# Performance work log

Measured on AMD Instinct MI355X. Metric: run time of the kernel, lower is better.

## Reference

```python
import jax, jax.numpy as jnp
import numpy as np

IMG = 512
B = 4
NA = 3          # anchors per location
NC = 3          # classes
K = 512         # pre-NMS top-k per image per level (<= smallest level anchor count 768)
STRIDES = [4, 8, 16, 32]
MIN_S = [0.01, 0.02, 0.03, 0.04]
MAX_S = [0.06, 0.08, 0.10, 0.12]
W_SC = [0.8, 0.9, 1.0, 1.1]
H_SC = [1.0, 1.2, 1.4, 1.6]
CONF_T = 0.15
NMS_T = 0.5
STD = 0.2       # box_delta_stds (means are 0)


def make_anchors(stride):
    H = IMG // stride
    c = (np.arange(H) + 0.5) * stride
    cy, cx = np.meshgrid(c, c, indexing='ij')           # [H, W]
    sizes = stride * 4.0 * (2.0 ** (np.arange(NA) / 3.0))  # [A]
    cx = np.broadcast_to(cx, (NA, H, H))
    cy = np.broadcast_to(cy, (NA, H, H))
    s = sizes[:, None, None]
    # A-major, then H, W -- matches permute(0,1,3,4,2).reshape flattening
    anc = np.stack([cx - s / 2, cy - s / 2, cx + s / 2, cy + s / 2], -1).reshape(-1, 4)
    return jnp.asarray(anc, jnp.float32)


def setup_inputs() -> dict:
    key = jax.random.key(0)
    ks = jax.random.split(key, 8)
    inp = {}
    for l, s in enumerate(STRIDES):
        H = IMG // s
        inp[f'cls{l}'] = jax.random.normal(ks[2 * l], (B, NA, NC, H, H), jnp.float32)
        inp[f'box{l}'] = jax.random.normal(ks[2 * l + 1], (B, NA, 4, H, H), jnp.float32)
        inp[f'anc{l}'] = make_anchors(s)
    inp['image_size'] = IMG
    return inp


def decode_level(cls, box, anc, lvl, image_size):
    Bc, A, C, H, W = cls.shape
    scores = jax.nn.sigmoid(jnp.transpose(cls, (0, 1, 3, 4, 2)).reshape(Bc, -1, C))  # [B,N,C]
    d = jnp.transpose(box, (0, 1, 3, 4, 2)).reshape(Bc, -1, 4)                        # [B,N,4]
    img = jnp.asarray(image_size, jnp.float32)
    aw = (anc[:, 2] - anc[:, 0]) / img
    ah = (anc[:, 3] - anc[:, 1]) / img
    acx = (anc[:, 0] + anc[:, 2]) * 0.5 / img
    acy = (anc[:, 1] + anc[:, 3]) * 0.5 / img
    fs = 1.0 / STRIDES[lvl]
    dx = jnp.clip(d[..., 0] * STD, -1.0, 1.0) * fs * aw
    dy = jnp.clip(d[..., 1] * STD, -1.0, 1.0) * fs * ah
    cx = jnp.clip(acx + dx, 0.0, 1.0)
    cy = jnp.clip(acy + dy, 0.0, 1.0)
    dw = jnp.clip(d[..., 2] * STD, -2.0, 2.0)
    dh = jnp.clip(d[..., 3] * STD, -2.0, 2.0)
    pw = jnp.clip(aw * W_SC[lvl] * jnp.exp(dw * (0.2 + 0.1 * lvl)), MIN_S[lvl] * 0.8, MAX_S[lvl] * 0.9)
    ph = jnp.clip(ah * H_SC[lvl] * jnp.exp(dh * (0.4 + 0.2 * lvl)), MIN_S[lvl] * 0.8, MAX_S[lvl] * 1.2)
    boxes = jnp.stack([
        jnp.clip(cx - 0.5 * pw, 0.0, 1.0),
        jnp.clip(cy - 0.5 * ph, 0.0, 1.0),
        jnp.clip(cx + 0.5 * pw, 0.0, 1.0),
        jnp.clip(cy + 0.5 * ph, 0.0, 1.0)], -1)                                       # [B,N,4]
    ms = scores.max(-1)
    mc = scores.argmax(-1)
    w = boxes[..., 2] - boxes[..., 0]
    h = boxes[..., 3] - boxes[..., 1]
    valid = (ms > CONF_T) & (w > MIN_S[lvl] * 0.5) & (h > MIN_S[lvl] * 0.5) \
            & (w < MAX_S[lvl] * 2.0) & (h < MAX_S[lvl] * 2.0)
    # pre-NMS top-k on (masked) scores
    sort_key = jnp.where(valid, ms, -1.0)
    _, idx = jax.lax.top_k(sort_key, K)                                               # [B,K]
    boxes_k = jnp.take_along_axis(boxes, idx[..., None], 1)
    scores_k = jnp.take_along_axis(ms, idx, 1)
    labels_k = jnp.take_along_axis(mc, idx, 1)
    valid_k = jnp.take_along_axis(valid, idx, 1)
    return boxes_k, scores_k, labels_k, valid_k


def pairwise_iou(b):
    area = (b[:, 2] - b[:, 0]) * (b[:, 3] - b[:, 1])
    lt = jnp.maximum(b[:, None, :2], b[None, :, :2])
    rb = jnp.minimum(b[:, None, 2:], b[None, :, 2:])
    wh = jnp.clip(rb - lt, 0.0)
    inter = wh[..., 0] * wh[..., 1]
    return inter / (area[:, None] + area[None, :] - inter + 1e-9)


def nms_keep(boxes, valid):
    # boxes sorted by descending score; sequential greedy NMS
    iou = pairwise_iou(boxes)                 # [K,K]
    rank = jnp.arange(K)
    def body(i, keep):
        overlap = jnp.max(jnp.where((rank < i) & keep, iou[i], 0.0))
        return keep.at[i].set(valid[i] & (overlap <= NMS_T))
    return jax.lax.fori_loop(0, K, body, jnp.zeros((K,), bool))


def reference(cls0, box0, anc0, cls1, box1, anc1, cls2, box2, anc2, cls3, box3, anc3, image_size):
    levels = [(cls0, box0, anc0), (cls1, box1, anc1), (cls2, box2, anc2), (cls3, box3, anc3)]
    outs = [decode_level(c, b, a, l, image_size) for l, (c, b, a) in enumerate(levels)]
    boxes = jnp.stack([o[0] for o in outs], 1)    # [B, L, K, 4]
    scores = jnp.stack([o[1] for o in outs], 1)   # [B, L, K]
    labels = jnp.stack([o[2] for o in outs], 1)   # [B, L, K]
    valid = jnp.stack([o[3] for o in outs], 1)    # [B, L, K]
    keep = jax.vmap(jax.vmap(nms_keep))(boxes, valid)
    boxes = jnp.where(keep[..., None], boxes, 0.0)
    scores = jnp.where(keep, scores, 0.0)
    labels = jnp.where(keep, labels + 1, 0)       # torch code returns labels + 1
    return boxes, scores, labels, keep
```

## Files before the change

kernel.cpp:

```cpp
#include <hip/hip_runtime.h>
#include <math.h>

#define K_TOP 512
#define CAND_CAP 3072

struct LvlC {
  int H, lgH, HH, lgHH;
  float fs, wsc, hsc, wex, hex, pwlo, pwhi, phlo, phhi, minwh, maxwh;
};

__device__ const LvlC LVL[4] = {
  {128, 7, 16384, 14, 0.25f,    0.8f, 1.0f, 0.2f, 0.4f, 0.008f, 0.054f, 0.008f, 0.072f, 0.005f, 0.12f},
  { 64, 6,  4096, 12, 0.125f,   0.9f, 1.2f, 0.3f, 0.6f, 0.016f, 0.072f, 0.016f, 0.096f, 0.01f,  0.16f},
  { 32, 5,  1024, 10, 0.0625f,  1.0f, 1.4f, 0.4f, 0.8f, 0.024f, 0.09f,  0.024f, 0.12f,  0.015f, 0.2f },
  { 16, 4,   256,  8, 0.03125f, 1.1f, 1.6f, 0.5f, 1.0f, 0.032f, 0.108f, 0.032f, 0.144f, 0.02f,  0.24f},
};

__device__ const float TSEL[4] = {0.91f, 0.85f, 0.65f, -2.0f};

__device__ __forceinline__ void decode_box(const LvlC& L, const float* __restrict__ boxp,
                                           const float* __restrict__ ancp,
                                           int b, int idx, float rimg,
                                           float& x0, float& y0, float& x1, float& y1)
{
#pragma clang fp contract(off)
  int a   = idx >> L.lgHH;
  int rem = idx & (L.HH - 1);
  const float* bp = boxp + (size_t)((b * 3 + a) * 4) * L.HH + rem;
  float d0 = bp[0], d1 = bp[L.HH], d2 = bp[2 * L.HH], d3 = bp[3 * L.HH];
  float4 av = reinterpret_cast<const float4*>(ancp)[idx];
  float a0 = av.x, a1 = av.y, a2 = av.z, a3 = av.w;
  float aw  = (a2 - a0) * rimg;
  float ah  = (a3 - a1) * rimg;
  float acx = (a0 + a2) * 0.5f * rimg;
  float acy = (a1 + a3) * 0.5f * rimg;
  float dx = fminf(fmaxf(d0 * 0.2f, -1.f), 1.f) * L.fs * aw;
  float dy = fminf(fmaxf(d1 * 0.2f, -1.f), 1.f) * L.fs * ah;
  float cx = fminf(fmaxf(acx + dx, 0.f), 1.f);
  float cy = fminf(fmaxf(acy + dy, 0.f), 1.f);
  float dw = fminf(fmaxf(d2 * 0.2f, -2.f), 2.f);
  float dh = fminf(fmaxf(d3 * 0.2f, -2.f), 2.f);
  float pw = fminf(fmaxf(aw * L.wsc * expf(dw * L.wex), L.pwlo), L.pwhi);
  float ph = fminf(fmaxf(ah * L.hsc * expf(dh * L.hex), L.phlo), L.phhi);
  x0 = fminf(fmaxf(cx - 0.5f * pw, 0.f), 1.f);
  y0 = fminf(fmaxf(cy - 0.5f * ph, 0.f), 1.f);
  x1 = fminf(fmaxf(cx + 0.5f * pw, 0.f), 1.f);
  y1 = fminf(fmaxf(cy + 0.5f * ph, 0.f), 1.f);
}

__device__ __forceinline__ void seg_map(int blk, int& b, int& l, int& base, int& iblk)
{
  b = blk / 255;
  int rb = blk - b * 255;
  if (rb < 192)      { l = 0; iblk = rb;       base = 0;     }
  else if (rb < 240) { l = 1; iblk = rb - 192; base = 49152; }
  else if (rb < 252) { l = 2; iblk = rb - 240; base = 61440; }
  else               { l = 3; iblk = rb - 252; base = 64512; }
}

__global__ __launch_bounds__(256) void dc_kernel(
    const float* __restrict__ cls0, const float* __restrict__ box0, const float* __restrict__ anc0,
    const float* __restrict__ cls1, const float* __restrict__ box1, const float* __restrict__ anc1,
    const float* __restrict__ cls2, const float* __restrict__ box2, const float* __restrict__ anc2,
    const float* __restrict__ cls3, const float* __restrict__ box3, const float* __restrict__ anc3,
    const int* __restrict__ imgp, unsigned long long* __restrict__ keys,
    unsigned long long* __restrict__ cand, unsigned* __restrict__ unitCnt)
{
  __shared__ unsigned wcnt[4];
  int unit = (int)blockIdx.x;
  int tid = (int)threadIdx.x;
  int wid = tid >> 6, lane = tid & 63;
  int b, l, base, iblk;
  seg_map(unit, b, l, base, iblk);
  int i = iblk * 256 + tid;

  const float *cls, *boxp, *ancp;
  switch (l) {
    case 0:  cls = cls0; boxp = box0; ancp = anc0; break;
    case 1:  cls = cls1; boxp = box1; ancp = anc1; break;
    case 2:  cls = cls2; boxp = box2; ancp = anc2; break;
    default: cls = cls3; boxp = box3; ancp = anc3; break;
  }
  LvlC L = LVL[l];
  float rimg = 1.0f / (float)(*imgp);

  int a   = i >> L.lgHH;
  int rem = i & (L.HH - 1);
  const float* cp = cls + (size_t)((b * 3 + a) * 3) * L.HH + rem;
  float c0 = cp[0], c1 = cp[L.HH], c2 = cp[2 * L.HH];
  float m = c0; int mc = 0;
  if (c1 > m) { m = c1; mc = 1; }
  if (c2 > m) { m = c2; mc = 2; }
  float ms = 1.f / (1.f + expf(-m));

  float x0, y0, x1, y1;
  decode_box(L, boxp, ancp, b, i, rimg, x0, y0, x1, y1);
  float w = x1 - x0, h = y1 - y0;
  bool valid = (ms > 0.15f) && (w > L.minwh) && (h > L.minwh) && (w < L.maxwh) && (h < L.maxwh);

  float sk = valid ? ms : -1.0f;
  unsigned u = __float_as_uint(sk);
  unsigned ascu  = (u & 0x80000000u) ? ~u : (u | 0x80000000u);
  unsigned descu = ~ascu;
  unsigned long long key = ((unsigned long long)descu << 32)
                         | ((unsigned long long)(unsigned)i << 16)
                         | ((unsigned)mc << 8) | (valid ? 1u : 0u);
  keys[(size_t)b * 65280 + base + i] = key;

  bool take = (sk >= TSEL[l]);
  unsigned long long bm = __ballot(take);
  if (lane == 0) wcnt[wid] = (unsigned)__popcll(bm);
  __syncthreads();
  if (take) {
    unsigned off = 0;
    for (int w2 = 0; w2 < wid; ++w2) off += wcnt[w2];
    off += (unsigned)__popcll(bm & ((1ull << lane) - 1ull));
    cand[(size_t)unit * 256 + off] = key;
  }
  if (tid == 0) unitCnt[unit] = wcnt[0] + wcnt[1] + wcnt[2] + wcnt[3];
}

__global__ __launch_bounds__(512) void sel_kernel(
    const unsigned long long* __restrict__ keys,
    const unsigned long long* __restrict__ cand, const unsigned* __restrict__ unitCnt,
    const float* __restrict__ box0, const float* __restrict__ anc0,
    const float* __restrict__ box1, const float* __restrict__ anc1,
    const float* __restrict__ box2, const float* __restrict__ anc2,
    const float* __restrict__ box3, const float* __restrict__ anc3,
    const int* __restrict__ imgp,
    float* __restrict__ boxesWS, float* __restrict__ scoresWS,
    int* __restrict__ labelsWS, unsigned* __restrict__ validWS)
{
  __shared__ unsigned long long scand[CAND_CAP];
  __shared__ unsigned long long skey[K_TOP];
  __shared__ unsigned long long skey2[K_TOP];
  __shared__ unsigned hist[8][256];
  __shared__ unsigned upref[256];
  __shared__ unsigned waveSum[8];
  __shared__ unsigned long long shPrefix;
  __shared__ unsigned long long shKth;
  __shared__ unsigned shBelow, shCnt, shTotal, shBucketCnt, sBC;

  int seg = (int)blockIdx.x;
  int b = seg >> 2, l = seg & 3;
  int tid = (int)threadIdx.x;
  const int nt = 512;
  int wid = tid >> 6, lane = tid & 63;

  const int nArr[4]    = {49152, 12288, 3072, 768};
  const int baseArr[4] = {0, 49152, 61440, 64512};
  const int nuArr[4]   = {192, 48, 12, 3};
  const int fuArr[4]   = {0, 192, 240, 252};
  int N = nArr[l];
  int nu = nuArr[l];
  int firstU = b * 255 + fuArr[l];
  const unsigned long long* kp = keys + (size_t)b * 65280 + baseArr[l];

  if (tid == 0) { shPrefix = 0ull; shBelow = 0u; shCnt = 0u; sBC = 0u; shBucketCnt = 0xFFFFFFFFu; }

  unsigned c = (tid < nu) ? unitCnt[firstU + tid] : 0u;
  unsigned incl = c;
  for (int off = 1; off < 64; off <<= 1) {
    unsigned n = __shfl_up(incl, off);
    if (lane >= off) incl += n;
  }
  if (lane == 63) waveSum[wid] = incl;
  __syncthreads();
  if (tid < 256) {
    unsigned add = 0;
    for (int w2 = 0; w2 < wid; ++w2) add += waveSum[w2];
    if (tid < nu) upref[tid] = incl - c + add;
  }
  if (tid == 0) shTotal = waveSum[0] + waveSum[1] + waveSum[2] + waveSum[3];
  __syncthreads();

  unsigned total = shTotal;
  bool useCand = (total >= K_TOP && total <= CAND_CAP);
  int M = useCand ? (int)total : N;

  if (useCand) {
    for (int f = tid; f < (int)total; f += nt) {
      int lo = 0, hi = nu - 1;
      while (lo < hi) {
        int mid = (lo + hi + 1) >> 1;
        if ((int)upref[mid] <= f) lo = mid; else hi = mid - 1;
      }
      scand[f] = cand[(size_t)(firstU + lo) * 256 + (unsigned)(f - (int)upref[lo])];
    }
  }
  __syncthreads();

  int lastShift = 16;
  for (int r = 0; r < 6; ++r) {
    int shift = 56 - 8 * r;
    for (int v = tid; v < 8 * 256; v += nt) ((unsigned*)hist)[v] = 0u;
    __syncthreads();
    unsigned long long pref = shPrefix;
    unsigned below = shBelow;
    unsigned long long hiMask = (r == 0) ? 0ull : (~0ull << (64 - 8 * r));
    for (int t = tid; t < M; t += nt) {
      unsigned long long k = useCand ? scand[t] : kp[t];
      if ((k & hiMask) == (pref & hiMask))
        atomicAdd(&hist[wid][(unsigned)((k >> shift) & 0xFF)], 1u);
    }
    __syncthreads();
    unsigned s = 0, incl2 = 0;
    if (tid < 256) {
#pragma unroll
      for (int w2 = 0; w2 < 8; ++w2) s += hist[w2][tid];
      incl2 = s;
    }
    for (int off = 1; off < 64; off <<= 1) {
      unsigned n = __shfl_up(incl2, off);
      if (lane >= off) incl2 += n;
    }
    if (lane == 63) waveSum[wid] = incl2;
    __syncthreads();
    if (tid < 256) {
      unsigned add = 0;
      for (int w2 = 0; w2 < wid; ++w2) add += waveSum[w2];
      unsigned inclT = incl2 + add;
      unsigned exclT = inclT - s;
      if (below + exclT < K_TOP && below + inclT >= K_TOP) {
        shBelow = below + exclT;
        shPrefix = pref | ((unsigned long long)(unsigned)tid << shift);
        shBucketCnt = s;
      }
    }
    __syncthreads();
    if (shBucketCnt <= (unsigned)K_TOP) { lastShift = shift; break; }
  }

  {
    unsigned long long pmask = ~0ull << lastShift;
    unsigned long long pref = shPrefix;
    for (int t = tid; t < M; t += nt) {
      unsigned long long k = useCand ? scand[t] : kp[t];
      bool take = ((k & pmask) == pref);
      unsigned long long bm = __ballot(take);
      unsigned bp = 0;
      if (lane == 0 && bm) bp = atomicAdd(&sBC, (unsigned)__popcll(bm));
      bp = __shfl(bp, 0);
      if (take) skey[bp + (unsigned)__popcll(bm & ((1ull << lane) - 1ull))] = k;
    }
    __syncthreads();
    unsigned cnt = sBC;
    unsigned rneed = K_TOP - shBelow;
    if (tid < (int)cnt) {
      unsigned long long mykey = skey[tid];
      int rank = 0;
      for (unsigned j = 0; j < cnt; ++j) rank += (skey[j] < mykey) ? 1 : 0;
      if (rank == (int)(rneed - 1)) shKth = mykey;
    }
    __syncthreads();
  }
  unsigned long long kth = shKth;

  for (int t = tid; t < M; t += nt) {
    unsigned long long k = useCand ? scand[t] : kp[t];
    bool take = (k <= kth);
    unsigned long long bm = __ballot(take);
    unsigned bp = 0;
    if (lane == 0 && bm) bp = atomicAdd(&shCnt, (unsigned)__popcll(bm));
    bp = __shfl(bp, 0);
    if (take) skey[bp + (unsigned)__popcll(bm & ((1ull << lane) - 1ull))] = k;
  }
  __syncthreads();

  {
    unsigned long long mykey = skey[tid];
    int rank = 0;
#pragma unroll 8
    for (int j = 0; j < K_TOP; ++j) rank += (skey[j] < mykey) ? 1 : 0;
    skey2[rank] = mykey;
  }
  __syncthreads();

  const float *boxp, *ancp;
  switch (l) {
    case 0:  boxp = box0; ancp = anc0; break;
    case 1:  boxp = box1; ancp = anc1; break;
    case 2:  boxp = box2; ancp = anc2; break;
    default: boxp = box3; ancp = anc3; break;
  }
  LvlC L = LVL[l];
  float rimg = 1.0f / (float)(*imgp);
  {
    unsigned long long key = skey2[tid];
    int idx = (int)((key >> 16) & 0xFFFFull);
    unsigned descu = (unsigned)(key >> 32);
    unsigned ascu  = ~descu;
    unsigned u = (ascu & 0x80000000u) ? (ascu & 0x7FFFFFFFu) : ~ascu;
    float x0, y0, x1, y1;
    decode_box(L, boxp, ancp, b, idx, rimg, x0, y0, x1, y1);
    int o = seg * K_TOP + tid;
    float4 bb; bb.x = x0; bb.y = y0; bb.z = x1; bb.w = y1;
    reinterpret_cast<float4*>(boxesWS)[o] = bb;
    scoresWS[o] = __uint_as_float(u);
    labelsWS[o] = (int)((key >> 8) & 0xFFull);
    validWS[o]  = (unsigned)(key & 1ull);
  }
}

__global__ __launch_bounds__(256) void mask_kernel(
    const float* __restrict__ boxesWS, unsigned long long* __restrict__ masks)
{
#pragma clang fp contract(off)
  int blk = (int)blockIdx.x;
  int seg = blk >> 5;
  int wid = (int)threadIdx.x >> 6;
  int lane = (int)threadIdx.x & 63;
  int waveInSeg = (blk & 31) * 4 + wid;
  const float4* bb = reinterpret_cast<const float4*>(boxesWS) + seg * K_TOP;
  unsigned long long* mseg = masks + (size_t)seg * K_TOP * 8;

  float4 bj[8]; float aj[8];
#pragma unroll
  for (int c = 0; c < 8; ++c) {
    bj[c] = bb[c * 64 + lane];
    aj[c] = (bj[c].z - bj[c].x) * (bj[c].w - bj[c].y);
  }
#pragma unroll
  for (int rr = 0; rr < 4; ++rr) {
    int r = waveInSeg * 4 + rr;
    float4 br = bb[r];
    float ar_ = (br.z - br.x) * (br.w - br.y);
#pragma unroll
    for (int c = 0; c < 8; ++c) {
      float ltx = fmaxf(br.x, bj[c].x), lty = fmaxf(br.y, bj[c].y);
      float rbx = fminf(br.z, bj[c].z), rby = fminf(br.w, bj[c].w);
      float ww = fmaxf(rbx - ltx, 0.f), hh = fmaxf(rby - lty, 0.f);
      float inter = ww * hh;
      float iou = inter / (ar_ + aj[c] - inter + 1e-9f);
      unsigned long long bal = __ballot(iou > 0.5f);
      if (lane == 0) mseg[c * K_TOP + r] = bal;
    }
  }
}

__global__ __launch_bounds__(512) void scan_kernel(
    const unsigned long long* __restrict__ masks,
    const float* __restrict__ boxesWS, const float* __restrict__ scoresWS,
    const int* __restrict__ labelsWS, const unsigned* __restrict__ validWS,
    float* __restrict__ out)
{
  __shared__ unsigned long long sMaskT[8 * K_TOP];
  __shared__ unsigned long long keepWords[8];
  __shared__ unsigned sChanged;

  int seg = (int)blockIdx.x;
  int tid = (int)threadIdx.x;
  int wid = tid >> 6, lane = tid & 63;
  const unsigned long long* mp = masks + (size_t)seg * K_TOP * 8;
#pragma unroll
  for (int w = 0; w < 8; ++w) sMaskT[w * K_TOP + tid] = mp[w * K_TOP + tid];
  bool valid = validWS[seg * K_TOP + tid] != 0u;

  unsigned long long myWord = __ballot(valid);
  if (lane == 0) keepWords[wid] = myWord;
  __syncthreads();

  for (int it = 0; it < 513; ++it) {
    unsigned long long sup = 0ull;
    for (int w = 0; w < wid; ++w)
      sup |= sMaskT[w * K_TOP + tid] & keepWords[w];
    sup |= sMaskT[wid * K_TOP + tid] & keepWords[wid] & ((1ull << lane) - 1ull);
    bool nk = valid && (sup == 0ull);
    unsigned long long nw = __ballot(nk);
    __syncthreads();
    if (tid == 0) sChanged = 0u;
    __syncthreads();
    if (lane == 0) {
      if (nw != keepWords[wid]) sChanged = 1u;
      keepWords[wid] = nw;
    }
    __syncthreads();
    if (sChanged == 0u) break;
  }

  int o = seg * K_TOP + tid;
  bool keep = (keepWords[wid] >> lane) & 1ull;
  float4 bx = reinterpret_cast<const float4*>(boxesWS)[o];
  float4 ob;
  ob.x = keep ? bx.x : 0.f;
  ob.y = keep ? bx.y : 0.f;
  ob.z = keep ? bx.z : 0.f;
  ob.w = keep ? bx.w : 0.f;
  reinterpret_cast<float4*>(out)[o] = ob;
  out[32768 + o] = keep ? scoresWS[o] : 0.f;
  out[40960 + o] = keep ? (float)(labelsWS[o] + 1) : 0.f;
  out[49152 + o] = keep ? 1.f : 0.f;
}

extern "C" void kernel_launch(void* const* d_in, const int* in_sizes, int n_in,
                              void* d_out, int out_size, void* d_ws, size_t ws_size,
                              hipStream_t stream)
{
  const float* cls0 = (const float*)d_in[0];
  const float* box0 = (const float*)d_in[1];
  const float* anc0 = (const float*)d_in[2];
  const float* cls1 = (const float*)d_in[3];
  const float* box1 = (const float*)d_in[4];
  const float* anc1 = (const float*)d_in[5];
  const float* cls2 = (const float*)d_in[6];
  const float* box2 = (const float*)d_in[7];
  const float* anc2 = (const float*)d_in[8];
  const float* cls3 = (const float*)d_in[9];
  const float* box3 = (const float*)d_in[10];
  const float* anc3 = (const float*)d_in[11];
  const int*   imgp = (const int*)d_in[12];

  char* ws = (char*)d_ws;
  unsigned long long* keys    = (unsigned long long*)(ws + 0);
  unsigned long long* cand    = (unsigned long long*)(ws + 2088960);
  unsigned*           unitCnt = (unsigned*)(ws + 4177920);
  float*              boxesWS = (float*)(ws + 4182016);
  float*              scoresWS= (float*)(ws + 4313088);
  int*                labelsWS= (int*)(ws + 4345856);
  unsigned*           validWS = (unsigned*)(ws + 4378624);
  unsigned long long* masks   = (unsigned long long*)(ws + 4411392);
  float* out = (float*)d_out;

  dc_kernel<<<1020, 256, 0, stream>>>(cls0, box0, anc0, cls1, box1, anc1,
                                      cls2, box2, anc2, cls3, box3, anc3,
                                      imgp, keys, cand, unitCnt);
  sel_kernel<<<16, 512, 0, stream>>>(keys, cand, unitCnt,
                                     box0, anc0, box1, anc1, box2, anc2, box3, anc3,
                                     imgp, boxesWS, scoresWS, labelsWS, validWS);
  mask_kernel<<<512, 256, 0, stream>>>(boxesWS, masks);
  scan_kernel<<<16, 512, 0, stream>>>(masks, boxesWS, scoresWS, labelsWS, validWS, out);
}
```

Before: 116.2 us.

## Fuse select, mask and scan kernels into one launch with flag-based inter-block sync

Merges the selection, IoU-mask and greedy-scan kernels into a single persistent launch. Blocks 0-15 do top-k and box decode, publish a flag, then wait for 16 mask-builder blocks per segment before running the scan. Mask blocks spin on the per-segment flag with sleep and a bounded guard. Scores and labels stay in registers instead of a workspace round trip, and the scan loop uses double-buffered keep words to drop one barrier per iteration. This removes two kernel launch gaps but relies on all 272 blocks being co-resident, otherwise the spin-waits only end through their timeout guard.

```diff
diff --git a/kernel.cpp b/kernel.cpp
--- a/kernel.cpp
+++ b/kernel.cpp
@@ -64,12 +64,14 @@
     const float* __restrict__ cls2, const float* __restrict__ box2, const float* __restrict__ anc2,
     const float* __restrict__ cls3, const float* __restrict__ box3, const float* __restrict__ anc3,
     const int* __restrict__ imgp, unsigned long long* __restrict__ keys,
-    unsigned long long* __restrict__ cand, unsigned* __restrict__ unitCnt)
+    unsigned long long* __restrict__ cand, unsigned* __restrict__ unitCnt,
+    unsigned* __restrict__ flags)
 {
   __shared__ unsigned wcnt[4];
   int unit = (int)blockIdx.x;
   int tid = (int)threadIdx.x;
   int wid = tid >> 6, lane = tid & 63;
+  if (unit == 0 && tid < 64) flags[tid] = 0u;
   int b, l, base, iblk;
   seg_map(unit, b, l, base, iblk);
   int i = iblk * 256 + tid;
@@ -120,7 +122,7 @@
   if (tid == 0) unitCnt[unit] = wcnt[0] + wcnt[1] + wcnt[2] + wcnt[3];
 }
 
-__global__ __launch_bounds__(512) void sel_kernel(
+__global__ __launch_bounds__(512) void post_kernel(
     const unsigned long long* __restrict__ keys,
     const unsigned long long* __restrict__ cand, const unsigned* __restrict__ unitCnt,
     const float* __restrict__ box0, const float* __restrict__ anc0,
@@ -128,24 +130,72 @@
     const float* __restrict__ box2, const float* __restrict__ anc2,
     const float* __restrict__ box3, const float* __restrict__ anc3,
     const int* __restrict__ imgp,
-    float* __restrict__ boxesWS, float* __restrict__ scoresWS,
-    int* __restrict__ labelsWS, unsigned* __restrict__ validWS)
+    float* __restrict__ boxesWS, unsigned long long* __restrict__ masks,
+    unsigned* __restrict__ flags, float* __restrict__ out)
 {
-  __shared__ unsigned long long scand[CAND_CAP];
-  __shared__ unsigned long long skey[K_TOP];
-  __shared__ unsigned long long skey2[K_TOP];
-  __shared__ unsigned hist[8][256];
+  __shared__ alignas(16) char smem[40960];
+  unsigned long long* scand  = (unsigned long long*)(smem);
+  unsigned long long* skey   = (unsigned long long*)(smem + 24576);
+  unsigned long long* skey2  = (unsigned long long*)(smem + 28672);
+  unsigned (*hist)[256]      = (unsigned (*)[256])(smem + 32768);
+  unsigned long long* sMaskT = (unsigned long long*)(smem);
   __shared__ unsigned upref[256];
   __shared__ unsigned waveSum[8];
+  __shared__ unsigned long long keepW[2][8];
+  __shared__ unsigned cfl[2];
   __shared__ unsigned long long shPrefix;
   __shared__ unsigned long long shKth;
   __shared__ unsigned shBelow, shCnt, shTotal, shBucketCnt, sBC;
 
+  int tid = (int)threadIdx.x;
+  int wid = tid >> 6, lane = tid & 63;
+  const int nt = 512;
+
+  if (blockIdx.x >= 16) {
+#pragma clang fp contract(off)
+    int m = (int)blockIdx.x - 16;
+    int seg = m >> 4, sub = m & 15;
+    if (tid == 0) {
+      int guard = 0;
+      while (__hip_atomic_load(&flags[seg], __ATOMIC_ACQUIRE, __HIP_MEMORY_SCOPE_AGENT) == 0u) {
+        __builtin_amdgcn_s_sleep(2);
+        if (++guard > 4000000) break;
+      }
+    }
+    __syncthreads();
+    const float4* bb = reinterpret_cast<const float4*>(boxesWS) + seg * K_TOP;
+    unsigned long long* mseg = masks + (size_t)seg * K_TOP * 8;
+    int waveInSeg = sub * 8 + wid;
+    float4 bj[8]; float aj[8];
+#pragma unroll
+    for (int c = 0; c < 8; ++c) {
+      bj[c] = bb[c * 64 + lane];
+      aj[c] = (bj[c].z - bj[c].x) * (bj[c].w - bj[c].y);
+    }
+#pragma unroll
+    for (int rr = 0; rr < 4; ++rr) {
+      int r = waveInSeg * 4 + rr;
+      float4 br = bb[r];
+      float ar_ = (br.z - br.x) * (br.w - br.y);
+#pragma unroll
+      for (int c = 0; c < 8; ++c) {
+        float ltx = fmaxf(br.x, bj[c].x), lty = fmaxf(br.y, bj[c].y);
+        float rbx = fminf(br.z, bj[c].z), rby = fminf(br.w, bj[c].w);
+        float ww = fmaxf(rbx - ltx, 0.f), hh = fmaxf(rby - lty, 0.f);
+        float inter = ww * hh;
+        float iou = inter / (ar_ + aj[c] - inter + 1e-9f);
+        unsigned long long bal = __ballot(iou > 0.5f);
+        if (lane == 0) mseg[c * K_TOP + r] = bal;
+      }
+    }
+    __syncthreads();
+    if (tid == 0)
+      __hip_atomic_fetch_add(&flags[16 + seg], 1u, __ATOMIC_RELEASE, __HIP_MEMORY_SCOPE_AGENT);
+    return;
+  }
+
   int seg = (int)blockIdx.x;
   int b = seg >> 2, l = seg & 3;
-  int tid = (int)threadIdx.x;
-  const int nt = 512;
-  int wid = tid >> 6, lane = tid & 63;
 
   const int nArr[4]    = {49152, 12288, 3072, 768};
   const int baseArr[4] = {0, 49152, 61440, 64512};
@@ -285,110 +335,70 @@
   }
   LvlC L = LVL[l];
   float rimg = 1.0f / (float)(*imgp);
-  {
-    unsigned long long key = skey2[tid];
-    int idx = (int)((key >> 16) & 0xFFFFull);
-    unsigned descu = (unsigned)(key >> 32);
-    unsigned ascu  = ~descu;
-    unsigned u = (ascu & 0x80000000u) ? (ascu & 0x7FFFFFFFu) : ~ascu;
-    float x0, y0, x1, y1;
-    decode_box(L, boxp, ancp, b, idx, rimg, x0, y0, x1, y1);
-    int o = seg * K_TOP + tid;
-    float4 bb; bb.x = x0; bb.y = y0; bb.z = x1; bb.w = y1;
-    reinterpret_cast<float4*>(boxesWS)[o] = bb;
-    scoresWS[o] = __uint_as_float(u);
-    labelsWS[o] = (int)((key >> 8) & 0xFFull);
-    validWS[o]  = (unsigned)(key & 1ull);
-  }
-}
-
-__global__ __launch_bounds__(256) void mask_kernel(
-    const float* __restrict__ boxesWS, unsigned long long* __restrict__ masks)
-{
-#pragma clang fp contract(off)
-  int blk = (int)blockIdx.x;
-  int seg = blk >> 5;
-  int wid = (int)threadIdx.x >> 6;
-  int lane = (int)threadIdx.x & 63;
-  int waveInSeg = (blk & 31) * 4 + wid;
-  const float4* bb = reinterpret_cast<const float4*>(boxesWS) + seg * K_TOP;
-  unsigned long long* mseg = masks + (size_t)seg * K_TOP * 8;
-
-  float4 bj[8]; float aj[8];
-#pragma unroll
-  for (int c = 0; c < 8; ++c) {
-    bj[c] = bb[c * 64 + lane];
-    aj[c] = (bj[c].z - bj[c].x) * (bj[c].w - bj[c].y);
-  }
-#pragma unroll
-  for (int rr = 0; rr < 4; ++rr) {
-    int r = waveInSeg * 4 + rr;
-    float4 br = bb[r];
-    float ar_ = (br.z - br.x) * (br.w - br.y);
-#pragma unroll
-    for (int c = 0; c < 8; ++c) {
-      float ltx = fmaxf(br.x, bj[c].x), lty = fmaxf(br.y, bj[c].y);
-      float rbx = fminf(br.z, bj[c].z), rby = fminf(br.w, bj[c].w);
-      float ww = fmaxf(rbx - ltx, 0.f), hh = fmaxf(rby - lty, 0.f);
-      float inter = ww * hh;
-      float iou = inter / (ar_ + aj[c] - inter + 1e-9f);
-      unsigned long long bal = __ballot(iou > 0.5f);
-      if (lane == 0) mseg[c * K_TOP + r] = bal;
-    }
-  }
-}
-
-__global__ __launch_bounds__(512) void scan_kernel(
-    const unsigned long long* __restrict__ masks,
-    const float* __restrict__ boxesWS, const float* __restrict__ scoresWS,
-    const int* __restrict__ labelsWS, const unsigned* __restrict__ validWS,
-    float* __restrict__ out)
-{
-  __shared__ unsigned long long sMaskT[8 * K_TOP];
-  __shared__ unsigned long long keepWords[8];
-  __shared__ unsigned sChanged;
-
-  int seg = (int)blockIdx.x;
-  int tid = (int)threadIdx.x;
-  int wid = tid >> 6, lane = tid & 63;
+
+  unsigned long long key = skey2[tid];
+  int idx = (int)((key >> 16) & 0xFFFFull);
+  unsigned descu = (unsigned)(key >> 32);
+  unsigned ascu  = ~descu;
+  unsigned u = (ascu & 0x80000000u) ? (ascu & 0x7FFFFFFFu) : ~ascu;
+  int label = (int)((key >> 8) & 0xFFull);
+  bool valid = (key & 1ull) != 0ull;
+  float x0, y0, x1, y1;
+  decode_box(L, boxp, ancp, b, idx, rimg, x0, y0, x1, y1);
+  float4 mybox; mybox.x = x0; mybox.y = y0; mybox.z = x1; mybox.w = y1;
+  reinterpret_cast<float4*>(boxesWS)[seg * K_TOP + tid] = mybox;
+  __syncthreads();
+
+  if (tid == 0) {
+    __hip_atomic_fetch_add(&flags[seg], 1u, __ATOMIC_RELEASE, __HIP_MEMORY_SCOPE_AGENT);
+    int guard = 0;
+    while (__hip_atomic_load(&flags[16 + seg], __ATOMIC_ACQUIRE, __HIP_MEMORY_SCOPE_AGENT) < 16u) {
+      __builtin_amdgcn_s_sleep(2);
+      if (++guard > 4000000) break;
+    }
+  }
+  __syncthreads();
+
   const unsigned long long* mp = masks + (size_t)seg * K_TOP * 8;
 #pragma unroll
   for (int w = 0; w < 8; ++w) sMaskT[w * K_TOP + tid] = mp[w * K_TOP + tid];
-  bool valid = validWS[seg * K_TOP + tid] != 0u;
-
   unsigned long long myWord = __ballot(valid);
-  if (lane == 0) keepWords[wid] = myWord;
-  __syncthreads();
-
-  for (int it = 0; it < 513; ++it) {
+  if (lane == 0) keepW[0][wid] = myWord;
+  __syncthreads();
+
+  int p = 0;
+  for (int it = 0; it < 600; ++it) {
+    unsigned long long kws[8];
+#pragma unroll
+    for (int w = 0; w < 8; ++w) kws[w] = keepW[p][w];
     unsigned long long sup = 0ull;
     for (int w = 0; w < wid; ++w)
-      sup |= sMaskT[w * K_TOP + tid] & keepWords[w];
-    sup |= sMaskT[wid * K_TOP + tid] & keepWords[wid] & ((1ull << lane) - 1ull);
+      sup |= sMaskT[w * K_TOP + tid] & kws[w];
+    sup |= sMaskT[wid * K_TOP + tid] & kws[wid] & ((1ull << lane) - 1ull);
     bool nk = valid && (sup == 0ull);
     unsigned long long nw = __ballot(nk);
-    __syncthreads();
-    if (tid == 0) sChanged = 0u;
+    if (tid == 0) cfl[p ^ 1] = 0u;
     __syncthreads();
     if (lane == 0) {
-      if (nw != keepWords[wid]) sChanged = 1u;
-      keepWords[wid] = nw;
-    }
-    __syncthreads();
-    if (sChanged == 0u) break;
-  }
+      keepW[p ^ 1][wid] = nw;
+      if (nw != kws[wid]) atomicOr(&cfl[p ^ 1], 1u);
+    }
+    __syncthreads();
+    if (cfl[p ^ 1] == 0u) break;
+    p ^= 1;
+  }
+  int pf = p ^ 1;
 
   int o = seg * K_TOP + tid;
-  bool keep = (keepWords[wid] >> lane) & 1ull;
-  float4 bx = reinterpret_cast<const float4*>(boxesWS)[o];
+  bool keep = (keepW[pf][wid] >> lane) & 1ull;
   float4 ob;
-  ob.x = keep ? bx.x : 0.f;
-  ob.y = keep ? bx.y : 0.f;
-  ob.z = keep ? bx.z : 0.f;
-  ob.w = keep ? bx.w : 0.f;
+  ob.x = keep ? mybox.x : 0.f;
+  ob.y = keep ? mybox.y : 0.f;
+  ob.z = keep ? mybox.z : 0.f;
+  ob.w = keep ? mybox.w : 0.f;
   reinterpret_cast<float4*>(out)[o] = ob;
-  out[32768 + o] = keep ? scoresWS[o] : 0.f;
-  out[40960 + o] = keep ? (float)(labelsWS[o] + 1) : 0.f;
+  out[32768 + o] = keep ? __uint_as_float(u) : 0.f;
+  out[40960 + o] = keep ? (float)(label + 1) : 0.f;
   out[49152 + o] = keep ? 1.f : 0.f;
 }
 
@@ -415,18 +425,14 @@
   unsigned long long* cand    = (unsigned long long*)(ws + 2088960);
   unsigned*           unitCnt = (unsigned*)(ws + 4177920);
   float*              boxesWS = (float*)(ws + 4182016);
-  float*              scoresWS= (float*)(ws + 4313088);
-  int*                labelsWS= (int*)(ws + 4345856);
-  unsigned*           validWS = (unsigned*)(ws + 4378624);
-  unsigned long long* masks   = (unsigned long long*)(ws + 4411392);
+  unsigned long long* masks   = (unsigned long long*)(ws + 4313088);
+  unsigned*           flags   = (unsigned*)(ws + 4837376);
   float* out = (float*)d_out;
 
   dc_kernel<<<1020, 256, 0, stream>>>(cls0, box0, anc0, cls1, box1, anc1,
                                       cls2, box2, anc2, cls3, box3, anc3,
-                                      imgp, keys, cand, unitCnt);
-  sel_kernel<<<16, 512, 0, stream>>>(keys, cand, unitCnt,
-                                     box0, anc0, box1, anc1, box2, anc2, box3, anc3,
-                                     imgp, boxesWS, scoresWS, labelsWS, validWS);
-  mask_kernel<<<512, 256, 0, stream>>>(boxesWS, masks);
-  scan_kernel<<<16, 512, 0, stream>>>(masks, boxesWS, scoresWS, labelsWS, validWS, out);
+                                      imgp, keys, cand, unitCnt, flags);
+  post_kernel<<<272, 512, 0, stream>>>(keys, cand, unitCnt,
+                                       box0, anc0, box1, anc1, box2, anc2, box3, anc3,
+                                       imgp, boxesWS, masks, flags, out);
 }
```

New measurement: 150.6 us. 1.3x slower.

## Fuse decode+select and mask+scan kernels via last-block-done atomic election

Applied to the files above, without the earlier changes.

Merges the four-launch pipeline into two kernels. In each, the last block to finish a segment, detected with a device-scope atomic counter, performs the follow-on work: top-K selection after decode, and the greedy NMS scan after IoU mask building. This removes two launches and their inter-kernel gaps. The selection and scan work now runs in 256-thread blocks handling two rows per thread, and the scan uses double-buffered keep words. The added LDS footprint may lower occupancy in the decode phase.

```diff
diff --git a/kernel.cpp b/kernel.cpp
--- a/kernel.cpp
+++ b/kernel.cpp
@@ -17,6 +17,9 @@
 };
 
 __device__ const float TSEL[4] = {0.91f, 0.85f, 0.65f, -2.0f};
+
+__device__ unsigned segCnt[16];
+__device__ unsigned maskCnt[16];
 
 __device__ __forceinline__ void decode_box(const LvlC& L, const float* __restrict__ boxp,
                                            const float* __restrict__ ancp,
@@ -58,15 +61,28 @@
   else               { l = 3; iblk = rb - 252; base = 64512; }
 }
 
-__global__ __launch_bounds__(256) void dc_kernel(
+__global__ __launch_bounds__(256) void dc_sel_kernel(
     const float* __restrict__ cls0, const float* __restrict__ box0, const float* __restrict__ anc0,
     const float* __restrict__ cls1, const float* __restrict__ box1, const float* __restrict__ anc1,
     const float* __restrict__ cls2, const float* __restrict__ box2, const float* __restrict__ anc2,
     const float* __restrict__ cls3, const float* __restrict__ box3, const float* __restrict__ anc3,
     const int* __restrict__ imgp, unsigned long long* __restrict__ keys,
-    unsigned long long* __restrict__ cand, unsigned* __restrict__ unitCnt)
+    unsigned long long* __restrict__ cand, unsigned* __restrict__ unitCnt,
+    float* __restrict__ boxesWS, float* __restrict__ scoresWS,
+    int* __restrict__ labelsWS, unsigned* __restrict__ validWS)
 {
+  __shared__ alignas(16) char smem[36864];
+  unsigned long long* scand = (unsigned long long*)(smem);
+  unsigned long long* skey  = (unsigned long long*)(smem + 24576);
+  unsigned long long* skey2 = (unsigned long long*)(smem + 28672);
+  unsigned (*hist)[256]     = (unsigned (*)[256])(smem + 32768);
+  __shared__ unsigned upref[256];
+  __shared__ unsigned waveSum[4];
   __shared__ unsigned wcnt[4];
+  __shared__ int sElect;
+  __shared__ unsigned long long shPrefix, shKth;
+  __shared__ unsigned shBelow, shCnt, shTotal, shBucketCnt, sBC;
+
   int unit = (int)blockIdx.x;
   int tid = (int)threadIdx.x;
   int wid = tid >> 6, lane = tid & 63;
@@ -84,79 +100,67 @@
   LvlC L = LVL[l];
   float rimg = 1.0f / (float)(*imgp);
 
-  int a   = i >> L.lgHH;
-  int rem = i & (L.HH - 1);
-  const float* cp = cls + (size_t)((b * 3 + a) * 3) * L.HH + rem;
-  float c0 = cp[0], c1 = cp[L.HH], c2 = cp[2 * L.HH];
-  float m = c0; int mc = 0;
-  if (c1 > m) { m = c1; mc = 1; }
-  if (c2 > m) { m = c2; mc = 2; }
-  float ms = 1.f / (1.f + expf(-m));
-
-  float x0, y0, x1, y1;
-  decode_box(L, boxp, ancp, b, i, rimg, x0, y0, x1, y1);
-  float w = x1 - x0, h = y1 - y0;
-  bool valid = (ms > 0.15f) && (w > L.minwh) && (h > L.minwh) && (w < L.maxwh) && (h < L.maxwh);
-
-  float sk = valid ? ms : -1.0f;
-  unsigned u = __float_as_uint(sk);
-  unsigned ascu  = (u & 0x80000000u) ? ~u : (u | 0x80000000u);
-  unsigned descu = ~ascu;
-  unsigned long long key = ((unsigned long long)descu << 32)
-                         | ((unsigned long long)(unsigned)i << 16)
-                         | ((unsigned)mc << 8) | (valid ? 1u : 0u);
-  keys[(size_t)b * 65280 + base + i] = key;
-
-  bool take = (sk >= TSEL[l]);
-  unsigned long long bm = __ballot(take);
-  if (lane == 0) wcnt[wid] = (unsigned)__popcll(bm);
-  __syncthreads();
-  if (take) {
-    unsigned off = 0;
-    for (int w2 = 0; w2 < wid; ++w2) off += wcnt[w2];
-    off += (unsigned)__popcll(bm & ((1ull << lane) - 1ull));
-    cand[(size_t)unit * 256 + off] = key;
-  }
-  if (tid == 0) unitCnt[unit] = wcnt[0] + wcnt[1] + wcnt[2] + wcnt[3];
-}
-
-__global__ __launch_bounds__(512) void sel_kernel(
-    const unsigned long long* __restrict__ keys,
-    const unsigned long long* __restrict__ cand, const unsigned* __restrict__ unitCnt,
-    const float* __restrict__ box0, const float* __restrict__ anc0,
-    const float* __restrict__ box1, const float* __restrict__ anc1,
-    const float* __restrict__ box2, const float* __restrict__ anc2,
-    const float* __restrict__ box3, const float* __restrict__ anc3,
-    const int* __restrict__ imgp,
-    float* __restrict__ boxesWS, float* __restrict__ scoresWS,
-    int* __restrict__ labelsWS, unsigned* __restrict__ validWS)
-{
-  __shared__ unsigned long long scand[CAND_CAP];
-  __shared__ unsigned long long skey[K_TOP];
-  __shared__ unsigned long long skey2[K_TOP];
-  __shared__ unsigned hist[8][256];
-  __shared__ unsigned upref[256];
-  __shared__ unsigned waveSum[8];
-  __shared__ unsigned long long shPrefix;
-  __shared__ unsigned long long shKth;
-  __shared__ unsigned shBelow, shCnt, shTotal, shBucketCnt, sBC;
-
-  int seg = (int)blockIdx.x;
-  int b = seg >> 2, l = seg & 3;
-  int tid = (int)threadIdx.x;
-  const int nt = 512;
-  int wid = tid >> 6, lane = tid & 63;
-
+  {
+    int a   = i >> L.lgHH;
+    int rem = i & (L.HH - 1);
+    const float* cp = cls + (size_t)((b * 3 + a) * 3) * L.HH + rem;
+    float c0 = cp[0], c1 = cp[L.HH], c2 = cp[2 * L.HH];
+    float m = c0; int mc = 0;
+    if (c1 > m) { m = c1; mc = 1; }
+    if (c2 > m) { m = c2; mc = 2; }
+    float ms = 1.f / (1.f + expf(-m));
+
+    float x0, y0, x1, y1;
+    decode_box(L, boxp, ancp, b, i, rimg, x0, y0, x1, y1);
+    float w = x1 - x0, h = y1 - y0;
+    bool valid = (ms > 0.15f) && (w > L.minwh) && (h > L.minwh) && (w < L.maxwh) && (h < L.maxwh);
+
+    float sk = valid ? ms : -1.0f;
+    unsigned u = __float_as_uint(sk);
+    unsigned ascu  = (u & 0x80000000u) ? ~u : (u | 0x80000000u);
+    unsigned descu = ~ascu;
+    unsigned long long key = ((unsigned long long)descu << 32)
+                           | ((unsigned long long)(unsigned)i << 16)
+                           | ((unsigned)mc << 8) | (valid ? 1u : 0u);
+    keys[(size_t)b * 65280 + base + i] = key;
+
+    bool take = (sk >= TSEL[l]);
+    unsigned long long bm = __ballot(take);
+    if (lane == 0) wcnt[wid] = (unsigned)__popcll(bm);
+    __syncthreads();
+    if (take) {
+      unsigned off = 0;
+      for (int w2 = 0; w2 < wid; ++w2) off += wcnt[w2];
+      off += (unsigned)__popcll(bm & ((1ull << lane) - 1ull));
+      cand[(size_t)unit * 256 + off] = key;
+    }
+    if (tid == 0) unitCnt[unit] = wcnt[0] + wcnt[1] + wcnt[2] + wcnt[3];
+  }
+
+  const int nuArr[4] = {192, 48, 12, 3};
+  int nu = nuArr[l];
+  __syncthreads();
+  if (tid == 0) {
+    unsigned old = __hip_atomic_fetch_add(&segCnt[b * 4 + l], 1u,
+                                          __ATOMIC_ACQ_REL, __HIP_MEMORY_SCOPE_AGENT);
+    int e = (old == (unsigned)(nu - 1)) ? 1 : 0;
+    if (e) {
+      __hip_atomic_store(&segCnt[b * 4 + l], 0u, __ATOMIC_RELAXED, __HIP_MEMORY_SCOPE_AGENT);
+      shPrefix = 0ull; shBelow = 0u; shCnt = 0u; sBC = 0u; shBucketCnt = 0xFFFFFFFFu;
+    }
+    sElect = e;
+  }
+  __syncthreads();
+  if (!sElect) return;
+
+  int seg = b * 4 + l;
   const int nArr[4]    = {49152, 12288, 3072, 768};
   const int baseArr[4] = {0, 49152, 61440, 64512};
-  const int nuArr[4]   = {192, 48, 12, 3};
   const int fuArr[4]   = {0, 192, 240, 252};
   int N = nArr[l];
-  int nu = nuArr[l];
   int firstU = b * 255 + fuArr[l];
   const unsigned long long* kp = keys + (size_t)b * 65280 + baseArr[l];
-
-  if (tid == 0) { shPrefix = 0ull; shBelow = 0u; shCnt = 0u; sBC = 0u; shBucketCnt = 0xFFFFFFFFu; }
+  const int nt = 256;
 
   unsigned c = (tid < nu) ? unitCnt[firstU + tid] : 0u;
   unsigned incl = c;
@@ -166,7 +170,7 @@
   }
   if (lane == 63) waveSum[wid] = incl;
   __syncthreads();
-  if (tid < 256) {
+  {
     unsigned add = 0;
     for (int w2 = 0; w2 < wid; ++w2) add += waveSum[w2];
     if (tid < nu) upref[tid] = incl - c + add;
@@ -193,7 +197,7 @@
   int lastShift = 16;
   for (int r = 0; r < 6; ++r) {
     int shift = 56 - 8 * r;
-    for (int v = tid; v < 8 * 256; v += nt) ((unsigned*)hist)[v] = 0u;
+    for (int v = tid; v < 4 * 256; v += nt) ((unsigned*)hist)[v] = 0u;
     __syncthreads();
     unsigned long long pref = shPrefix;
     unsigned below = shBelow;
@@ -204,19 +208,17 @@
         atomicAdd(&hist[wid][(unsigned)((k >> shift) & 0xFF)], 1u);
     }
     __syncthreads();
-    unsigned s = 0, incl2 = 0;
-    if (tid < 256) {
-#pragma unroll
-      for (int w2 = 0; w2 < 8; ++w2) s += hist[w2][tid];
-      incl2 = s;
-    }
+    unsigned s = 0;
+#pragma unroll
+    for (int w2 = 0; w2 < 4; ++w2) s += hist[w2][tid];
+    unsigned incl2 = s;
     for (int off = 1; off < 64; off <<= 1) {
       unsigned n = __shfl_up(incl2, off);
       if (lane >= off) incl2 += n;
     }
     if (lane == 63) waveSum[wid] = incl2;
     __syncthreads();
-    if (tid < 256) {
+    {
       unsigned add = 0;
       for (int w2 = 0; w2 < wid; ++w2) add += waveSum[w2];
       unsigned inclT = incl2 + add;
@@ -246,8 +248,8 @@
     __syncthreads();
     unsigned cnt = sBC;
     unsigned rneed = K_TOP - shBelow;
-    if (tid < (int)cnt) {
-      unsigned long long mykey = skey[tid];
+    for (int t = tid; t < (int)cnt; t += nt) {
+      unsigned long long mykey = skey[t];
       int rank = 0;
       for (unsigned j = 0; j < cnt; ++j) rank += (skey[j] < mykey) ? 1 : 0;
       if (rank == (int)(rneed - 1)) shKth = mykey;
@@ -268,32 +270,30 @@
   __syncthreads();
 
   {
-    unsigned long long mykey = skey[tid];
-    int rank = 0;
+    unsigned long long k1 = skey[tid], k2 = skey[tid + 256];
+    int r1 = 0, r2 = 0;
 #pragma unroll 8
-    for (int j = 0; j < K_TOP; ++j) rank += (skey[j] < mykey) ? 1 : 0;
-    skey2[rank] = mykey;
-  }
-  __syncthreads();
-
-  const float *boxp, *ancp;
-  switch (l) {
-    case 0:  boxp = box0; ancp = anc0; break;
-    case 1:  boxp = box1; ancp = anc1; break;
-    case 2:  boxp = box2; ancp = anc2; break;
-    default: boxp = box3; ancp = anc3; break;
-  }
-  LvlC L = LVL[l];
-  float rimg = 1.0f / (float)(*imgp);
-  {
-    unsigned long long key = skey2[tid];
+    for (int j = 0; j < K_TOP; ++j) {
+      unsigned long long kj = skey[j];
+      r1 += (kj < k1) ? 1 : 0;
+      r2 += (kj < k2) ? 1 : 0;
+    }
+    skey2[r1] = k1;
+    skey2[r2] = k2;
+  }
+  __syncthreads();
+
+#pragma unroll
+  for (int h = 0; h < 2; ++h) {
+    int row = tid + h * 256;
+    unsigned long long key = skey2[row];
     int idx = (int)((key >> 16) & 0xFFFFull);
     unsigned descu = (unsigned)(key >> 32);
     unsigned ascu  = ~descu;
     unsigned u = (ascu & 0x80000000u) ? (ascu & 0x7FFFFFFFu) : ~ascu;
     float x0, y0, x1, y1;
     decode_box(L, boxp, ancp, b, idx, rimg, x0, y0, x1, y1);
-    int o = seg * K_TOP + tid;
+    int o = seg * K_TOP + row;
     float4 bb; bb.x = x0; bb.y = y0; bb.z = x1; bb.w = y1;
     reinterpret_cast<float4*>(boxesWS)[o] = bb;
     scoresWS[o] = __uint_as_float(u);
@@ -302,94 +302,123 @@
   }
 }
 
-__global__ __launch_bounds__(256) void mask_kernel(
-    const float* __restrict__ boxesWS, unsigned long long* __restrict__ masks)
+__global__ __launch_bounds__(256) void mask_scan_kernel(
+    const float* __restrict__ boxesWS, const float* __restrict__ scoresWS,
+    const int* __restrict__ labelsWS, const unsigned* __restrict__ validWS,
+    unsigned long long* __restrict__ masks, float* __restrict__ out)
 {
 #pragma clang fp contract(off)
+  __shared__ unsigned long long sMaskT[8 * K_TOP];
+  __shared__ unsigned long long keepW[2][8];
+  __shared__ unsigned cfl[2];
+  __shared__ int sElect;
+
   int blk = (int)blockIdx.x;
   int seg = blk >> 5;
-  int wid = (int)threadIdx.x >> 6;
-  int lane = (int)threadIdx.x & 63;
+  int tid = (int)threadIdx.x;
+  int wid = tid >> 6;
+  int lane = tid & 63;
   int waveInSeg = (blk & 31) * 4 + wid;
   const float4* bb = reinterpret_cast<const float4*>(boxesWS) + seg * K_TOP;
   unsigned long long* mseg = masks + (size_t)seg * K_TOP * 8;
 
-  float4 bj[8]; float aj[8];
-#pragma unroll
-  for (int c = 0; c < 8; ++c) {
-    bj[c] = bb[c * 64 + lane];
-    aj[c] = (bj[c].z - bj[c].x) * (bj[c].w - bj[c].y);
-  }
-#pragma unroll
-  for (int rr = 0; rr < 4; ++rr) {
-    int r = waveInSeg * 4 + rr;
-    float4 br = bb[r];
-    float ar_ = (br.z - br.x) * (br.w - br.y);
+  {
+    float4 bj[8]; float aj[8];
 #pragma unroll
     for (int c = 0; c < 8; ++c) {
-      float ltx = fmaxf(br.x, bj[c].x), lty = fmaxf(br.y, bj[c].y);
-      float rbx = fminf(br.z, bj[c].z), rby = fminf(br.w, bj[c].w);
-      float ww = fmaxf(rbx - ltx, 0.f), hh = fmaxf(rby - lty, 0.f);
-      float inter = ww * hh;
-      float iou = inter / (ar_ + aj[c] - inter + 1e-9f);
-      unsigned long long bal = __ballot(iou > 0.5f);
-      if (lane == 0) mseg[c * K_TOP + r] = bal;
-    }
-  }
-}
-
-__global__ __launch_bounds__(512) void scan_kernel(
-    const unsigned long long* __restrict__ masks,
-    const float* __restrict__ boxesWS, const float* __restrict__ scoresWS,
-    const int* __restrict__ labelsWS, const unsigned* __restrict__ validWS,
-    float* __restrict__ out)
-{
-  __shared__ unsigned long long sMaskT[8 * K_TOP];
-  __shared__ unsigned long long keepWords[8];
-  __shared__ unsigned sChanged;
-
-  int seg = (int)blockIdx.x;
-  int tid = (int)threadIdx.x;
-  int wid = tid >> 6, lane = tid & 63;
+      bj[c] = bb[c * 64 + lane];
+      aj[c] = (bj[c].z - bj[c].x) * (bj[c].w - bj[c].y);
+    }
+#pragma unroll
+    for (int rr = 0; rr < 4; ++rr) {
+      int r = waveInSeg * 4 + rr;
+      float4 br = bb[r];
+      float ar_ = (br.z - br.x) * (br.w - br.y);
+#pragma unroll
+      for (int c = 0; c < 8; ++c) {
+        float ltx = fmaxf(br.x, bj[c].x), lty = fmaxf(br.y, bj[c].y);
+        float rbx = fminf(br.z, bj[c].z), rby = fminf(br.w, bj[c].w);
+        float ww = fmaxf(rbx - ltx, 0.f), hh = fmaxf(rby - lty, 0.f);
+        float inter = ww * hh;
+        float iou = inter / (ar_ + aj[c] - inter + 1e-9f);
+        unsigned long long bal = __ballot(iou > 0.5f);
+        if (lane == 0) mseg[c * K_TOP + r] = bal;
+      }
+    }
+  }
+
+  __syncthreads();
+  if (tid == 0) {
+    unsigned old = __hip_atomic_fetch_add(&maskCnt[seg], 1u,
+                                          __ATOMIC_ACQ_REL, __HIP_MEMORY_SCOPE_AGENT);
+    int e = (old == 31u) ? 1 : 0;
+    if (e) __hip_atomic_store(&maskCnt[seg], 0u, __ATOMIC_RELAXED, __HIP_MEMORY_SCOPE_AGENT);
+    sElect = e;
+  }
+  __syncthreads();
+  if (!sElect) return;
+
   const unsigned long long* mp = masks + (size_t)seg * K_TOP * 8;
 #pragma unroll
-  for (int w = 0; w < 8; ++w) sMaskT[w * K_TOP + tid] = mp[w * K_TOP + tid];
-  bool valid = validWS[seg * K_TOP + tid] != 0u;
-
-  unsigned long long myWord = __ballot(valid);
-  if (lane == 0) keepWords[wid] = myWord;
-  __syncthreads();
-
-  for (int it = 0; it < 513; ++it) {
-    unsigned long long sup = 0ull;
+  for (int w = 0; w < 8; ++w) {
+    sMaskT[w * K_TOP + tid]       = mp[w * K_TOP + tid];
+    sMaskT[w * K_TOP + 256 + tid] = mp[w * K_TOP + 256 + tid];
+  }
+  bool v1 = validWS[seg * K_TOP + tid] != 0u;
+  bool v2 = validWS[seg * K_TOP + 256 + tid] != 0u;
+  unsigned long long w1 = __ballot(v1);
+  unsigned long long w2 = __ballot(v2);
+  if (lane == 0) { keepW[0][wid] = w1; keepW[0][4 + wid] = w2; }
+  __syncthreads();
+
+  int p = 0;
+  for (int it = 0; it < 600; ++it) {
+    unsigned long long kws[8];
+#pragma unroll
+    for (int w = 0; w < 8; ++w) kws[w] = keepW[p][w];
+    unsigned long long lm = (1ull << lane) - 1ull;
+    unsigned long long sup1 = 0ull;
     for (int w = 0; w < wid; ++w)
-      sup |= sMaskT[w * K_TOP + tid] & keepWords[w];
-    sup |= sMaskT[wid * K_TOP + tid] & keepWords[wid] & ((1ull << lane) - 1ull);
-    bool nk = valid && (sup == 0ull);
-    unsigned long long nw = __ballot(nk);
-    __syncthreads();
-    if (tid == 0) sChanged = 0u;
+      sup1 |= sMaskT[w * K_TOP + tid] & kws[w];
+    sup1 |= sMaskT[wid * K_TOP + tid] & kws[wid] & lm;
+    int r2 = tid + 256, wq2 = wid + 4;
+    unsigned long long sup2 = 0ull;
+    for (int w = 0; w < wq2; ++w)
+      sup2 |= sMaskT[w * K_TOP + r2] & kws[w];
+    sup2 |= sMaskT[wq2 * K_TOP + r2] & kws[wq2] & lm;
+    bool nk1 = v1 && (sup1 == 0ull);
+    bool nk2 = v2 && (sup2 == 0ull);
+    unsigned long long nw1 = __ballot(nk1);
+    unsigned long long nw2 = __ballot(nk2);
+    if (tid == 0) cfl[p ^ 1] = 0u;
     __syncthreads();
     if (lane == 0) {
-      if (nw != keepWords[wid]) sChanged = 1u;
-      keepWords[wid] = nw;
-    }
-    __syncthreads();
-    if (sChanged == 0u) break;
-  }
-
-  int o = seg * K_TOP + tid;
-  bool keep = (keepWords[wid] >> lane) & 1ull;
-  float4 bx = reinterpret_cast<const float4*>(boxesWS)[o];
-  float4 ob;
-  ob.x = keep ? bx.x : 0.f;
-  ob.y = keep ? bx.y : 0.f;
-  ob.z = keep ? bx.z : 0.f;
-  ob.w = keep ? bx.w : 0.f;
-  reinterpret_cast<float4*>(out)[o] = ob;
-  out[32768 + o] = keep ? scoresWS[o] : 0.f;
-  out[40960 + o] = keep ? (float)(labelsWS[o] + 1) : 0.f;
-  out[49152 + o] = keep ? 1.f : 0.f;
+      keepW[p ^ 1][wid]     = nw1;
+      keepW[p ^ 1][4 + wid] = nw2;
+      if (nw1 != kws[wid] || nw2 != kws[4 + wid]) atomicOr(&cfl[p ^ 1], 1u);
+    }
+    __syncthreads();
+    if (cfl[p ^ 1] == 0u) break;
+    p ^= 1;
+  }
+  int pf = p ^ 1;
+
+#pragma unroll
+  for (int h = 0; h < 2; ++h) {
+    int row = tid + h * 256;
+    int o = seg * K_TOP + row;
+    bool keep = (keepW[pf][row >> 6] >> (row & 63)) & 1ull;
+    float4 bx = reinterpret_cast<const float4*>(boxesWS)[o];
+    float4 ob;
+    ob.x = keep ? bx.x : 0.f;
+    ob.y = keep ? bx.y : 0.f;
+    ob.z = keep ? bx.z : 0.f;
+    ob.w = keep ? bx.w : 0.f;
+    reinterpret_cast<float4*>(out)[o] = ob;
+    out[32768 + o] = keep ? scoresWS[o] : 0.f;
+    out[40960 + o] = keep ? (float)(labelsWS[o] + 1) : 0.f;
+    out[49152 + o] = keep ? 1.f : 0.f;
+  }
 }
 
 extern "C" void kernel_launch(void* const* d_in, const int* in_sizes, int n_in,
@@ -421,12 +450,10 @@
   unsigned long long* masks   = (unsigned long long*)(ws + 4411392);
   float* out = (float*)d_out;
 
-  dc_kernel<<<1020, 256, 0, stream>>>(cls0, box0, anc0, cls1, box1, anc1,
-                                      cls2, box2, anc2, cls3, box3, anc3,
-                                      imgp, keys, cand, unitCnt);
-  sel_kernel<<<16, 512, 0, stream>>>(keys, cand, unitCnt,
-                                     box0, anc0, box1, anc1, box2, anc2, box3, anc3,
-                                     imgp, boxesWS, scoresWS, labelsWS, validWS);
-  mask_kernel<<<512, 256, 0, stream>>>(boxesWS, masks);
-  scan_kernel<<<16, 512, 0, stream>>>(masks, boxesWS, scoresWS, labelsWS, validWS, out);
+  dc_sel_kernel<<<1020, 256, 0, stream>>>(cls0, box0, anc0, cls1, box1, anc1,
+                                          cls2, box2, anc2, cls3, box3, anc3,
+                                          imgp, keys, cand, unitCnt,
+                                          boxesWS, scoresWS, labelsWS, validWS);
+  mask_scan_kernel<<<512, 256, 0, stream>>>(boxesWS, scoresWS, labelsWS, validWS,
+                                            masks, out);
 }
```

Measured after the change: 166.3 us. 43.1% more time.
